# Kernel optimization log

Measured on AMD Instinct MI355X. Metric: run time of the kernel, lower is better.

Reference implementation:

```python
import jax, jax.numpy as jnp
import numpy as np

# hyperparameters (module defaults)
T, B, N = 200, 64, 4096
TAU = 20.0
DT = 1.0
ETA = 0.1
NOISE_STD = 0.1
V_RESET = 0.0
MIN_TH = 0.5
MAX_TH = 2.0
ADAPT_DECAY = 0.9
SPIKE_INC = 0.5
DEP_RATE = 0.1
REC_RATE = 0.05


def setup_inputs() -> dict:
    key = jax.random.key(0)
    input_data = jax.random.normal(key, (T, B, N), dtype=jnp.float32)
    return {
        "input_data": input_data,
        "V0": jnp.zeros((B, N), jnp.float32),
        "V_th0": jnp.ones((B, N), jnp.float32),
        "adaptation0": jnp.zeros((B, N), jnp.float32),
        "syn_eff0": jnp.ones((B, N), jnp.float32),
        "neuromod0": jnp.zeros((B, N), jnp.float32),
    }


def _run(input_data, V0, V_th0, adaptation0, syn_eff0, neuromod0):
    # Deterministic per-step PRNG keys for noise + Bernoulli spike sampling.
    keys = jax.random.split(jax.random.key(42), input_data.shape[0])

    def step(carry, xs):
        V, Vth, adapt, syn = carry
        I, k = xs
        k_noise, k_spike = jax.random.split(k)
        noise = jax.random.normal(k_noise, I.shape, I.dtype) * NOISE_STD
        # effective input current with synaptic efficiency, neuromodulation, adaptation
        I_eff = I * syn + neuromod0 - adapt
        V = V + (I_eff - V) * (DT / TAU) + noise
        # stochastic spiking: sigmoid probability, Bernoulli sample
        spike_prob = jax.nn.sigmoid(V - Vth)
        spikes = jax.random.uniform(k_spike, V.shape, V.dtype) < spike_prob
        V = jnp.where(spikes, V_RESET, V)
        # adaptive threshold: bump on spike, relax toward 1.0 otherwise
        Vth = jnp.where(spikes, Vth + ETA, Vth - ETA * (Vth - 1.0))
        Vth = jnp.clip(Vth, MIN_TH, MAX_TH)
        sf = spikes.astype(V.dtype)
        adapt = adapt * ADAPT_DECAY + SPIKE_INC * sf
        syn = syn * (1.0 - DEP_RATE * sf) + REC_RATE * (1.0 - syn)
        return (V, Vth, adapt, syn), (spikes, V)

    _, (out_spikes, voltages) = jax.lax.scan(
        step, (V0, V_th0, adaptation0, syn_eff0), (input_data, keys)
    )
    return out_spikes, voltages  # (T,B,N) bool, (T,B,N) float


def reference(input_data, V0, V_th0, adaptation0, syn_eff0, neuromod0):
    return _run(input_data, V0, V_th0, adaptation0, syn_eff0, neuromod0)
```

## Files before the change

### kernel.cpp

```cpp
#include <hip/hip_runtime.h>
#include <stdint.h>


#define TSTEPS 200
#define BN     262144u
#define TBN    ((size_t)TSTEPS * (size_t)BN)

__device__ __forceinline__ void tf2x32(uint32_t k0, uint32_t k1,
                                       uint32_t c0, uint32_t c1,
                                       uint32_t& o0, uint32_t& o1) {
  uint32_t ks2 = k0 ^ k1 ^ 0x1BD11BDAu;
  uint32_t x0 = c0 + k0, x1 = c1 + k1;
#define R1(r) { x0 += x1; x1 = (x1 << (r)) | (x1 >> (32 - (r))); x1 ^= x0; }
#define R4A R1(13) R1(15) R1(26) R1(6)
#define R4B R1(17) R1(29) R1(16) R1(24)
  R4A; x0 += k1;  x1 += ks2 + 1u;
  R4B; x0 += ks2; x1 += k0 + 2u;
  R4A; x0 += k0;  x1 += k1 + 3u;
  R4B; x0 += k1;  x1 += ks2 + 4u;
  R4A; x0 += ks2; x1 += k0 + 5u;
#undef R4A
#undef R4B
#undef R1
  o0 = x0; o1 = x1;
}

__device__ __forceinline__ float erfinv_f32(float x) {
#pragma clang fp contract(off)
  float w = -log1pf(-(x * x));
  float p;
  if (w < 5.0f) {
    w = w - 2.5f;
    p =  2.81022636e-08f;
    p =  3.43273939e-07f + p * w;
    p = -3.5233877e-06f  + p * w;
    p = -4.39150654e-06f + p * w;
    p =  0.00021858087f  + p * w;
    p = -0.00125372503f  + p * w;
    p = -0.00417768164f  + p * w;
    p =  0.246640727f    + p * w;
    p =  1.50140941f     + p * w;
  } else {
    w = sqrtf(w) - 3.0f;
    p = -0.000200214257f;
    p =  0.000100950558f + p * w;
    p =  0.00134934322f  + p * w;
    p = -0.00367342844f  + p * w;
    p =  0.00573950773f  + p * w;
    p = -0.0076224613f   + p * w;
    p =  0.00943887047f  + p * w;
    p =  1.00167406f     + p * w;
    p =  2.83297682f     + p * w;
  }
  return p * x;
}

__device__ __forceinline__ float u01(uint32_t b) {
#pragma clang fp contract(off)
  return __uint_as_float((b >> 9) | 0x3f800000u) - 1.0f;
}

__global__ void keys_kernel(uint4* __restrict__ gK) {
  int t = blockIdx.x * blockDim.x + threadIdx.x;
  if (t >= TSTEPS) return;
  uint32_t K0, K1; tf2x32(0u, 42u, 0u, (uint32_t)t, K0, K1);
  uint32_t n0, n1; tf2x32(K0, K1, 0u, 0u, n0, n1);
  uint32_t s0, s1; tf2x32(K0, K1, 0u, 1u, s0, s1);
  gK[t] = make_uint4(n0, n1, s0, s1);
}

__global__ __launch_bounds__(256) void lif_kernel(
    const float* __restrict__ gI,
    const float* __restrict__ gV0, const float* __restrict__ gT0,
    const float* __restrict__ gA0, const float* __restrict__ gS0,
    const float* __restrict__ gN0,
    const uint4* __restrict__ gK,
    float* __restrict__ gOut)
{
#pragma clang fp contract(off)
  __shared__ uint4 kt[TSTEPS];
  for (int i = threadIdx.x; i < TSTEPS; i += 256) kt[i] = gK[i];
  __syncthreads();

  const uint32_t e = blockIdx.x * 256u + threadIdx.x;
  const float LO = -0x1.fffffep-1f;
  const float SQRT2 = 1.4142135623730951f;

  float V  = gV0[e];
  float Th = gT0[e];
  float Ad = gA0[e];
  float Sy = gS0[e];
  float Nm = gN0[e];

  const float* Ip = gI + e;
  float* So = gOut + e;
  float* Vo = gOut + TBN + e;

  for (int t = 0; t < TSTEPS; ++t) {
    uint4 k = kt[t];
    size_t off = (size_t)t * BN;
    float I = Ip[off];

    uint32_t b0, b1; tf2x32(k.x, k.y, 0u, e, b0, b1);
    float un = u01(b0 ^ b1);
    float x = un * 2.0f + LO;
    x = fmaxf(LO, x);
    float nrm = SQRT2 * erfinv_f32(x);
    float noise = nrm * 0.1f;

    float Ieff = (I * Sy + Nm) - Ad;
    V = (V + (Ieff - V) * 0.05f) + noise;

    float d = V - Th;
    float ex = expf(-d);
    float p = 1.0f / (1.0f + ex);

    uint32_t c0, c1; tf2x32(k.z, k.w, 0u, e, c0, c1);
    float us = u01(c0 ^ c1);
    us = fmaxf(0.0f, us);
    bool spk = us < p;
    float sf = spk ? 1.0f : 0.0f;

    V = spk ? 0.0f : V;
    float thn = Th - 0.1f * (Th - 1.0f);
    Th = spk ? (Th + 0.1f) : thn;
    Th = fminf(fmaxf(Th, 0.5f), 2.0f);
    Ad = Ad * 0.9f + 0.5f * sf;
    Sy = Sy * (1.0f - 0.1f * sf) + 0.05f * (1.0f - Sy);

    So[off] = sf;
    Vo[off] = V;
  }
}

extern "C" void kernel_launch(void* const* d_in, const int* in_sizes, int n_in,
                              void* d_out, int out_size, void* d_ws, size_t ws_size,
                              hipStream_t stream) {
  const float* I    = (const float*)d_in[0];
  const float* V0   = (const float*)d_in[1];
  const float* Vth0 = (const float*)d_in[2];
  const float* ad0  = (const float*)d_in[3];
  const float* sy0  = (const float*)d_in[4];
  const float* nm0  = (const float*)d_in[5];
  float* out = (float*)d_out;
  uint4* ktab = (uint4*)d_ws;

  keys_kernel<<<1, 256, 0, stream>>>(ktab);
  lif_kernel<<<BN / 256, 256, 0, stream>>>(I, V0, Vth0, ad0, sy0, nm0, ktab, out);
}
```

Measured before the change: 853.3 us.

## Software-pipeline RNG and input loads one step ahead, use scalar keys and nontemporal stores

The time loop now computes the noise and uniform values and loads the input for step t+1 while step t's recurrence is evaluated. This lets the independent RNG work and global loads overlap the serial dependency chain. The LDS key table and barrier are replaced by per-step global loads whose values are made wave-uniform with readfirstlane. Output stores are made nontemporal to avoid polluting the cache. It costs more live registers and adds a peeled final iteration.

New measurement: 848.8 us. About the same (-0.5%).

```diff
diff --git a/kernel.cpp b/kernel.cpp
--- a/kernel.cpp
+++ b/kernel.cpp
@@ -60,6 +60,24 @@
   return __uint_as_float((b >> 9) | 0x3f800000u) - 1.0f;
 }
 
+__device__ __forceinline__ float noise_from(uint32_t k0, uint32_t k1, uint32_t e) {
+#pragma clang fp contract(off)
+  const float LO = -0x1.fffffep-1f;
+  const float SQRT2 = 1.4142135623730951f;
+  uint32_t b0, b1; tf2x32(k0, k1, 0u, e, b0, b1);
+  float un = u01(b0 ^ b1);
+  float x = un * 2.0f + LO;
+  x = fmaxf(LO, x);
+  float nrm = SQRT2 * erfinv_f32(x);
+  return nrm * 0.1f;
+}
+
+__device__ __forceinline__ float us_from(uint32_t k0, uint32_t k1, uint32_t e) {
+#pragma clang fp contract(off)
+  uint32_t c0, c1; tf2x32(k0, k1, 0u, e, c0, c1);
+  return fmaxf(0.0f, u01(c0 ^ c1));
+}
+
 __global__ void keys_kernel(uint4* __restrict__ gK) {
   int t = blockIdx.x * blockDim.x + threadIdx.x;
   if (t >= TSTEPS) return;
@@ -78,13 +96,7 @@
     float* __restrict__ gOut)
 {
 #pragma clang fp contract(off)
-  __shared__ uint4 kt[TSTEPS];
-  for (int i = threadIdx.x; i < TSTEPS; i += 256) kt[i] = gK[i];
-  __syncthreads();
-
   const uint32_t e = blockIdx.x * 256u + threadIdx.x;
-  const float LO = -0x1.fffffep-1f;
-  const float SQRT2 = 1.4142135623730951f;
 
   float V  = gV0[e];
   float Th = gT0[e];
@@ -96,29 +108,33 @@
   float* So = gOut + e;
   float* Vo = gOut + TBN + e;
 
-  for (int t = 0; t < TSTEPS; ++t) {
-    uint4 k = kt[t];
-    size_t off = (size_t)t * BN;
-    float I = Ip[off];
+  uint4 kk0 = gK[0];
+  uint32_t a0 = __builtin_amdgcn_readfirstlane(kk0.x);
+  uint32_t a1 = __builtin_amdgcn_readfirstlane(kk0.y);
+  uint32_t a2 = __builtin_amdgcn_readfirstlane(kk0.z);
+  uint32_t a3 = __builtin_amdgcn_readfirstlane(kk0.w);
+  float noise_c = noise_from(a0, a1, e);
+  float us_c    = us_from(a2, a3, e);
+  float I_c     = Ip[0];
+  Ip += BN;
 
-    uint32_t b0, b1; tf2x32(k.x, k.y, 0u, e, b0, b1);
-    float un = u01(b0 ^ b1);
-    float x = un * 2.0f + LO;
-    x = fmaxf(LO, x);
-    float nrm = SQRT2 * erfinv_f32(x);
-    float noise = nrm * 0.1f;
+  for (int t = 0; t < TSTEPS - 1; ++t) {
+    uint4 kk = gK[t + 1];
+    uint32_t k0 = __builtin_amdgcn_readfirstlane(kk.x);
+    uint32_t k1 = __builtin_amdgcn_readfirstlane(kk.y);
+    uint32_t k2 = __builtin_amdgcn_readfirstlane(kk.z);
+    uint32_t k3 = __builtin_amdgcn_readfirstlane(kk.w);
+    float noise_n = noise_from(k0, k1, e);
+    float us_n    = us_from(k2, k3, e);
+    float I_n     = Ip[0];
+    Ip += BN;
 
-    float Ieff = (I * Sy + Nm) - Ad;
-    V = (V + (Ieff - V) * 0.05f) + noise;
-
-    float d = V - Th;
-    float ex = expf(-d);
+    float Ieff = (I_c * Sy + Nm) - Ad;
+    V = (V + (Ieff - V) * 0.05f) + noise_c;
+    float md = Th - V;
+    float ex = expf(md);
     float p = 1.0f / (1.0f + ex);
-
-    uint32_t c0, c1; tf2x32(k.z, k.w, 0u, e, c0, c1);
-    float us = u01(c0 ^ c1);
-    us = fmaxf(0.0f, us);
-    bool spk = us < p;
+    bool spk = us_c < p;
     float sf = spk ? 1.0f : 0.0f;
 
     V = spk ? 0.0f : V;
@@ -128,8 +144,24 @@
     Ad = Ad * 0.9f + 0.5f * sf;
     Sy = Sy * (1.0f - 0.1f * sf) + 0.05f * (1.0f - Sy);
 
-    So[off] = sf;
-    Vo[off] = V;
+    __builtin_nontemporal_store(sf, So);
+    __builtin_nontemporal_store(V,  Vo);
+    So += BN; Vo += BN;
+
+    noise_c = noise_n; us_c = us_n; I_c = I_n;
+  }
+
+  {
+    float Ieff = (I_c * Sy + Nm) - Ad;
+    V = (V + (Ieff - V) * 0.05f) + noise_c;
+    float md = Th - V;
+    float ex = expf(md);
+    float p = 1.0f / (1.0f + ex);
+    bool spk = us_c < p;
+    float sf = spk ? 1.0f : 0.0f;
+    V = spk ? 0.0f : V;
+    __builtin_nontemporal_store(sf, So);
+    __builtin_nontemporal_store(V,  Vo);
   }
 }
 
```

## Split RNG generation into a fully parallel pre-pass, prefetch in the scan

Applied to the files above, without the earlier changes.

Noise and uniform samples for every timestep are now computed by a separate 2D-grid kernel and written into the output buffer, so the sequential scan kernel only reads them back. This exposes the Threefry and erfinv work across T×BN threads instead of 1024 blocks looping 200 times. The scan kernel software-prefetches inputs two steps ahead and uses nontemporal stores. In exchange it adds a full extra write and read of two T×B×N float arrays, and the scan overwrites its own inputs in place.

After: 925.3 us. 8.4% more time.

```diff
diff --git a/kernel.cpp b/kernel.cpp
--- a/kernel.cpp
+++ b/kernel.cpp
@@ -69,22 +69,45 @@
   gK[t] = make_uint4(n0, n1, s0, s1);
 }
 
-__global__ __launch_bounds__(256) void lif_kernel(
+__global__ __launch_bounds__(256) void gen_kernel(
+    const uint4* __restrict__ gK, float* __restrict__ gOut)
+{
+#pragma clang fp contract(off)
+  const uint32_t t = blockIdx.y;
+  const uint32_t e = blockIdx.x * 256u + threadIdx.x;
+
+  uint4 kk = gK[t];
+  uint32_t k0 = __builtin_amdgcn_readfirstlane(kk.x);
+  uint32_t k1 = __builtin_amdgcn_readfirstlane(kk.y);
+  uint32_t k2 = __builtin_amdgcn_readfirstlane(kk.z);
+  uint32_t k3 = __builtin_amdgcn_readfirstlane(kk.w);
+
+  const float LO = -0x1.fffffep-1f;
+  const float SQRT2 = 1.4142135623730951f;
+
+  uint32_t b0, b1; tf2x32(k0, k1, 0u, e, b0, b1);
+  float un = u01(b0 ^ b1);
+  float x = un * 2.0f + LO;
+  x = fmaxf(LO, x);
+  float noise = (SQRT2 * erfinv_f32(x)) * 0.1f;
+
+  uint32_t c0, c1; tf2x32(k2, k3, 0u, e, c0, c1);
+  float us = fmaxf(0.0f, u01(c0 ^ c1));
+
+  size_t off = (size_t)t * BN + e;
+  gOut[off] = noise;
+  gOut[TBN + off] = us;
+}
+
+__global__ __launch_bounds__(256) void scan_kernel(
     const float* __restrict__ gI,
     const float* __restrict__ gV0, const float* __restrict__ gT0,
     const float* __restrict__ gA0, const float* __restrict__ gS0,
     const float* __restrict__ gN0,
-    const uint4* __restrict__ gK,
-    float* __restrict__ gOut)
+    float* gOut)
 {
 #pragma clang fp contract(off)
-  __shared__ uint4 kt[TSTEPS];
-  for (int i = threadIdx.x; i < TSTEPS; i += 256) kt[i] = gK[i];
-  __syncthreads();
-
   const uint32_t e = blockIdx.x * 256u + threadIdx.x;
-  const float LO = -0x1.fffffep-1f;
-  const float SQRT2 = 1.4142135623730951f;
 
   float V  = gV0[e];
   float Th = gT0[e];
@@ -93,32 +116,25 @@
   float Nm = gN0[e];
 
   const float* Ip = gI + e;
-  float* So = gOut + e;
-  float* Vo = gOut + TBN + e;
+  float* Op = gOut + e;
+  float* Up = gOut + TBN + e;
+
+  float I0 = Ip[0],          N0 = Op[0],          U0 = Up[0];
+  float I1 = Ip[(size_t)BN], N1 = Op[(size_t)BN], U1 = Up[(size_t)BN];
 
   for (int t = 0; t < TSTEPS; ++t) {
-    uint4 k = kt[t];
-    size_t off = (size_t)t * BN;
-    float I = Ip[off];
+    float I2 = 0.0f, N2 = 0.0f, U2 = 0.0f;
+    if (t + 2 < TSTEPS) {
+      size_t pf = (size_t)(t + 2) * BN;
+      I2 = Ip[pf]; N2 = Op[pf]; U2 = Up[pf];
+    }
 
-    uint32_t b0, b1; tf2x32(k.x, k.y, 0u, e, b0, b1);
-    float un = u01(b0 ^ b1);
-    float x = un * 2.0f + LO;
-    x = fmaxf(LO, x);
-    float nrm = SQRT2 * erfinv_f32(x);
-    float noise = nrm * 0.1f;
-
-    float Ieff = (I * Sy + Nm) - Ad;
-    V = (V + (Ieff - V) * 0.05f) + noise;
-
-    float d = V - Th;
-    float ex = expf(-d);
+    float Ieff = (I0 * Sy + Nm) - Ad;
+    V = (V + (Ieff - V) * 0.05f) + N0;
+    float md = Th - V;
+    float ex = expf(md);
     float p = 1.0f / (1.0f + ex);
-
-    uint32_t c0, c1; tf2x32(k.z, k.w, 0u, e, c0, c1);
-    float us = u01(c0 ^ c1);
-    us = fmaxf(0.0f, us);
-    bool spk = us < p;
+    bool spk = U0 < p;
     float sf = spk ? 1.0f : 0.0f;
 
     V = spk ? 0.0f : V;
@@ -128,8 +144,12 @@
     Ad = Ad * 0.9f + 0.5f * sf;
     Sy = Sy * (1.0f - 0.1f * sf) + 0.05f * (1.0f - Sy);
 
-    So[off] = sf;
-    Vo[off] = V;
+    size_t so = (size_t)t * BN;
+    __builtin_nontemporal_store(sf, Op + so);
+    __builtin_nontemporal_store(V,  Up + so);
+
+    I0 = I1; N0 = N1; U0 = U1;
+    I1 = I2; N1 = N2; U1 = U2;
   }
 }
 
@@ -146,5 +166,6 @@
   uint4* ktab = (uint4*)d_ws;
 
   keys_kernel<<<1, 256, 0, stream>>>(ktab);
-  lif_kernel<<<BN / 256, 256, 0, stream>>>(I, V0, Vth0, ad0, sy0, nm0, ktab, out);
+  gen_kernel<<<dim3(BN / 256, TSTEPS), 256, 0, stream>>>(ktab, out);
+  scan_kernel<<<BN / 256, 256, 0, stream>>>(I, V0, Vth0, ad0, sy0, nm0, out);
 }
```
